# Optimization experiments

Measured on AMD Instinct MI355X. Metric: run time of the kernel, lower is better.

The kernel has to match this reference:

```python
import jax, jax.numpy as jnp
import numpy as np

B, V, H = 16384, 1024, 256


def setup_inputs() -> dict:
    key = jax.random.key(0)
    k1, k2 = jax.random.split(key)
    # binary spin configurations in {0,1}
    batch = jax.random.bernoulli(k1, 0.5, (B, V)).astype(jnp.float32)
    # small weights + negative hidden bias keep exp(log p*) finite in fp32
    weights_amp = jax.random.normal(k2, (H, V), dtype=jnp.float32) * (0.05 / np.sqrt(V))
    visible_bias_amp = jnp.zeros((V,), dtype=jnp.float32)
    hidden_bias_amp = -5.0 * jnp.ones((H,), dtype=jnp.float32)
    return {
        'batch': batch,
        'weights_amp': weights_amp,
        'visible_bias_amp': visible_bias_amp,
        'hidden_bias_amp': hidden_bias_amp,
        'k': 8,
    }


def _gibbs_sampling_amp(v0, W, vb, hb, k, key):
    """k steps of block Gibbs sampling, vectorized over the whole batch [B,V]."""
    keys = jax.random.split(key, 2 * k).reshape(k, 2)

    def step(v, ks):
        ph = jax.nn.sigmoid(v @ W.T + hb)                      # [B,H]
        h = (jax.random.uniform(ks[0], ph.shape) < ph).astype(v.dtype)
        pv = jax.nn.sigmoid(h @ W + vb)                        # [B,V]
        v = (jax.random.uniform(ks[1], pv.shape) < pv).astype(v.dtype)
        return v, None

    vk, _ = jax.lax.scan(step, v0, keys)
    return vk


def reference(batch, weights_amp, visible_bias_amp, hidden_bias_amp, k):
    W, vb, hb = weights_amp, visible_bias_amp, hidden_bias_amp
    nbatch = batch.shape[0]
    key = jax.random.key(42)

    vk = _gibbs_sampling_amp(batch, W, vb, hb, k, key)          # [B,V]

    ph0 = jax.nn.sigmoid(batch @ W.T + hb)                      # [B,H] positive-phase hidden probs
    pre_k = vk @ W.T + hb                                       # [B,H]
    phk = jax.nn.sigmoid(pre_k)                                 # [B,H] negative-phase hidden probs

    # unnormalized_probability_amp(vk) = exp(vk.vb + sum_j softplus((W vk + hb)_j))
    log_p = vk @ vb + jax.nn.softplus(pre_k).sum(axis=-1)       # [B]
    inv_norm = jnp.exp(-log_p) / nbatch                         # 1 / (len(batch) * p*(vk))

    # g_W = sum_b [outer(phk_b, vk_b) - outer(ph0_b, v0_b)] / norm_b
    g_w = (jnp.einsum('b,bh,bv->hv', inv_norm, phk, vk)
           - jnp.einsum('b,bh,bv->hv', inv_norm, ph0, batch))   # [H,V]
    g_vb = jnp.einsum('b,bv->v', inv_norm, vk - batch)          # [V]
    g_hb = jnp.einsum('b,bh->h', inv_norm, phk - ph0)           # [H]

    return jnp.concatenate([g_w.ravel(), g_vb, g_hb])
```

## Files before the change

kernel.cpp:

```cpp
#include <hip/hip_runtime.h>
#include <stdint.h>

#define B_DIM 16384
#define V_DIM 1024
#define H_DIM 256
#define K_STEPS 8

typedef short bf16x8 __attribute__((ext_vector_type(8)));
typedef float f32x4 __attribute__((ext_vector_type(4)));

__host__ __device__ inline uint32_t rotl32(uint32_t v, int r) {
#if defined(__HIP_DEVICE_COMPILE__)
    return __builtin_amdgcn_alignbit(v, v, (uint32_t)(32 - r));
#else
    return (v << r) | (v >> (32 - r));
#endif
}

__host__ __device__ inline void threefry2x32(uint32_t k0, uint32_t k1,
                                             uint32_t x0, uint32_t x1,
                                             uint32_t* o0, uint32_t* o1) {
    uint32_t k2 = k0 ^ k1 ^ 0x1BD11BDAu;
    x0 += k0; x1 += k1;
#define TF_RND(r) { x0 += x1; x1 = rotl32(x1, (r)); x1 ^= x0; }
    TF_RND(13) TF_RND(15) TF_RND(26) TF_RND(6)
    x0 += k1; x1 += k2 + 1u;
    TF_RND(17) TF_RND(29) TF_RND(16) TF_RND(24)
    x0 += k2; x1 += k0 + 2u;
    TF_RND(13) TF_RND(15) TF_RND(26) TF_RND(6)
    x0 += k0; x1 += k1 + 3u;
    TF_RND(17) TF_RND(29) TF_RND(16) TF_RND(24)
    x0 += k1; x1 += k2 + 4u;
    TF_RND(13) TF_RND(15) TF_RND(26) TF_RND(6)
    x0 += k2; x1 += k0 + 5u;
#undef TF_RND
    *o0 = x0; *o1 = x1;
}

__device__ inline float tf_uniform(uint32_t key0, uint32_t key1, uint32_t e) {
    uint32_t o0, o1;
    threefry2x32(key0, key1, 0u, e, &o0, &o1);
    uint32_t bits = o0 ^ o1;
    return __uint_as_float((bits >> 9) | 0x3f800000u) - 1.0f;
}

__device__ inline uint16_t bf16_rn(float f) {
    uint32_t u = __float_as_uint(f);
    uint32_t r = u + 0x7FFFu + ((u >> 16) & 1u);
    return (uint16_t)(r >> 16);
}
__device__ inline float bf16_to_f32(uint16_t h) {
    return __uint_as_float(((uint32_t)h) << 16);
}

__device__ inline void gload_lds16(const void* g, void* l) {
    __builtin_amdgcn_global_load_lds((const __attribute__((address_space(1))) uint32_t*)g,
                                     (__attribute__((address_space(3))) uint32_t*)l, 16, 0, 0);
}

struct KeyPack { uint32_t hk0[8], hk1[8], vk0[8], vk1[8]; };

__global__ __launch_bounds__(512, 4) void gibbs_fused(
    const ushort* __restrict__ batch_bf,
    const ushort* __restrict__ Whi, const ushort* __restrict__ Wlo,
    const float* __restrict__ Wf, const float* __restrict__ vb,
    const float* __restrict__ hb, ushort* __restrict__ v_cur,
    ushort* __restrict__ ph0b, ushort* __restrict__ phkb, KeyPack kp) {
    __shared__ __align__(16) ushort As[2][32 * 32];
    __shared__ __align__(16) ushort BhS[2][256 * 32];
    __shared__ __align__(16) ushort BlS[2][256 * 32];

    const int tid = threadIdx.x;
    const int lane = tid & 63;
    const int w = tid >> 6;
    const int m0 = blockIdx.x * 32;

    const int wm = (w & 1) * 16;
    const int wn = (w >> 1) * 64;
    const int q = lane >> 4;
    const int l15 = lane & 15;
    const int srow = lane >> 2;
    const int scol = (lane & 3) * 8;

    ushort* h_lds = &BhS[0][0];

    for (int step = 0; step <= K_STEPS; ++step) {
        const ushort* Asrc = (step == 0) ? batch_bf : v_cur;
        f32x4 acc[4] = {};

        for (int k0 = 0; k0 < V_DIM; k0 += 64) {
            if (w < 4) {
                const int s = w & 1, rh = w >> 1;
                gload_lds16(&Asrc[(size_t)(m0 + rh * 16 + srow) * V_DIM + k0 + s * 32 + scol],
                            &As[s][rh * 512]);
            }
#pragma unroll
            for (int c = 0; c < 4; ++c) {
                const int cc = w + 8 * c;
                const int s = cc & 1, rb = cc >> 1;
                const size_t off = (size_t)(rb * 16 + srow) * V_DIM + k0 + s * 32 + scol;
                gload_lds16(&Whi[off], &BhS[s][rb * 512]);
                gload_lds16(&Wlo[off], &BlS[s][rb * 512]);
            }
            __syncthreads();
#pragma unroll
            for (int s = 0; s < 2; ++s) {
                bf16x8 af = *(const bf16x8*)&As[s][(wm + l15) * 32 + q * 8];
#pragma unroll
                for (int j = 0; j < 4; ++j) {
                    bf16x8 bh = *(const bf16x8*)&BhS[s][(wn + j * 16 + l15) * 32 + q * 8];
                    bf16x8 bl = *(const bf16x8*)&BlS[s][(wn + j * 16 + l15) * 32 + q * 8];
                    acc[j] = __builtin_amdgcn_mfma_f32_16x16x32_bf16(af, bh, acc[j], 0, 0, 0);
                    acc[j] = __builtin_amdgcn_mfma_f32_16x16x32_bf16(af, bl, acc[j], 0, 0, 0);
                }
            }
            __syncthreads();
        }

        if (step == K_STEPS) {
#pragma unroll
            for (int j = 0; j < 4; ++j) {
                const int col = wn + j * 16 + l15;
                const float hbv = hb[col];
#pragma unroll
                for (int r = 0; r < 4; ++r) {
                    const int row = m0 + wm + q * 4 + r;
                    float val = acc[j][r] + hbv;
                    phkb[(size_t)row * H_DIM + col] = bf16_rn(1.0f / (1.0f + expf(-val)));
                }
            }
            break;
        }

        const uint32_t kh0 = kp.hk0[step], kh1 = kp.hk1[step];
#pragma unroll
        for (int j = 0; j < 4; ++j) {
            const int col = wn + j * 16 + l15;
            const float hbv = hb[col];
#pragma unroll
            for (int r = 0; r < 4; ++r) {
                const int rowl = wm + q * 4 + r;
                const int row = m0 + rowl;
                float val = acc[j][r] + hbv;
                float E = expf(-val);
                float u = tf_uniform(kh0, kh1, (uint32_t)row * (uint32_t)H_DIM + (uint32_t)col);
                h_lds[rowl * H_DIM + col] = (fmaf(u, E, u) < 1.0f) ? (ushort)0x3F80 : (ushort)0;
                if (step == 0) {
                    ph0b[(size_t)row * H_DIM + col] = bf16_rn(1.0f / (1.0f + E));
                }
            }
        }
        __syncthreads();

        const uint32_t kv0 = kp.vk0[step], kv1 = kp.vk1[step];
        float vbr[16];
#pragma unroll
        for (int t = 0; t < 16; ++t) vbr[t] = vb[lane + 64 * t];
#pragma unroll
        for (int rr = 0; rr < 4; ++rr) {
            const int bl_ = w * 4 + rr;
            const int b = m0 + bl_;
            ushort4 hv = ((const ushort4*)(h_lds + bl_ * H_DIM))[lane];
            unsigned long long masks[4];
            masks[0] = __ballot(hv.x != 0);
            masks[1] = __ballot(hv.y != 0);
            masks[2] = __ballot(hv.z != 0);
            masks[3] = __ballot(hv.w != 0);

            float acc2[16];
#pragma unroll
            for (int t = 0; t < 16; ++t) acc2[t] = 0.0f;

#pragma unroll
            for (int s = 0; s < 4; ++s) {
                unsigned long long m = masks[s];
                while (m) {
                    int l = __ffsll(m) - 1;
                    m &= m - 1;
                    int jj = l * 4 + s;
                    const float* wrow = Wf + (size_t)jj * V_DIM + lane;
#pragma unroll
                    for (int t = 0; t < 16; ++t) acc2[t] += wrow[64 * t];
                }
            }

            const uint32_t ebase = (uint32_t)b * (uint32_t)V_DIM + (uint32_t)lane;
            ushort* orow = v_cur + (size_t)b * V_DIM + lane;
#pragma unroll
            for (int t = 0; t < 16; ++t) {
                float pre = acc2[t] + vbr[t];
                float E = expf(-pre);
                float u = tf_uniform(kv0, kv1, ebase + 64u * (uint32_t)t);
                orow[64 * t] = (fmaf(u, E, u) < 1.0f) ? (ushort)0x3F80 : (ushort)0;
            }
        }
        __syncthreads();
    }
}

__global__ __launch_bounds__(256, 4) void mfma_gemm_acc(
    const ushort* __restrict__ A, const ushort* __restrict__ Bt,
    float* __restrict__ out, int N, int K, int k_slice) {
    __shared__ __align__(16) ushort As[64 * 32];
    __shared__ __align__(16) ushort Bs[64 * 32];

    const int tid = threadIdx.x;
    const int lane = tid & 63;
    const int w = tid >> 6;
    const int m0 = blockIdx.x * 64;
    const int n0 = blockIdx.y * 64;
    const int kbase = blockIdx.z * k_slice;

    f32x4 acc[2][2] = {};

    const int wm = (w & 1) * 32;
    const int wn = (w >> 1) * 32;
    const int q = lane >> 4;
    const int l15 = lane & 15;
    const int srow = lane >> 2;
    const int scol = (lane & 3) * 8;

    const size_t arow = (size_t)(m0 + w * 16 + srow) * K;
    const size_t brow = (size_t)(n0 + w * 16 + srow) * K;

    for (int kt = 0; kt < k_slice; kt += 32) {
        const int k0 = kbase + kt;
        gload_lds16(&A[arow + k0 + scol], &As[w * 512]);
        gload_lds16(&Bt[brow + k0 + scol], &Bs[w * 512]);
        __syncthreads();
        bf16x8 af[2], bf[2];
#pragma unroll
        for (int i = 0; i < 2; ++i) {
            af[i] = *(const bf16x8*)&As[(wm + i * 16 + l15) * 32 + q * 8];
            bf[i] = *(const bf16x8*)&Bs[(wn + i * 16 + l15) * 32 + q * 8];
        }
#pragma unroll
        for (int i = 0; i < 2; ++i)
#pragma unroll
            for (int j = 0; j < 2; ++j)
                acc[i][j] = __builtin_amdgcn_mfma_f32_16x16x32_bf16(af[i], bf[j], acc[i][j], 0, 0, 0);
        __syncthreads();
    }

    const int orow = q * 4;
#pragma unroll
    for (int i = 0; i < 2; ++i)
#pragma unroll
        for (int j = 0; j < 2; ++j) {
            int col = n0 + wn + j * 16 + l15;
#pragma unroll
            for (int r = 0; r < 4; ++r) {
                int row = m0 + wm + i * 16 + orow + r;
                atomicAdd(&out[(size_t)row * N + col], acc[i][j][r]);
            }
        }
}

__global__ void wsplit_kernel(const float* __restrict__ W, ushort* __restrict__ whi,
                              ushort* __restrict__ wlo) {
    int idx = blockIdx.x * 256 + threadIdx.x;
    float w = W[idx];
    ushort hi = bf16_rn(w);
    float fhi = bf16_to_f32(hi);
    ushort lo = bf16_rn(w - fhi);
    whi[idx] = hi; wlo[idx] = lo;
}

__global__ void tobf16_kernel(const float* __restrict__ src, ushort* __restrict__ dst) {
    int idx = blockIdx.x * 256 + threadIdx.x;
    float4 f = ((const float4*)src)[idx];
    ushort4 o;
    o.x = bf16_rn(f.x); o.y = bf16_rn(f.y); o.z = bf16_rn(f.z); o.w = bf16_rn(f.w);
    ((ushort4*)dst)[idx] = o;
}

__global__ __launch_bounds__(256) void lognorm_kernel(
    const ushort* __restrict__ phk, const ushort* __restrict__ vk,
    const float* __restrict__ vb, float* __restrict__ inv) {
    int b = blockIdx.x;
    int tid = threadIdx.x;
    float p = bf16_to_f32(phk[(size_t)b * H_DIM + tid]);
    float s = -log1pf(-p);
    for (int j = tid; j < V_DIM; j += 256)
        s += bf16_to_f32(vk[(size_t)b * V_DIM + j]) * vb[j];
    for (int off = 32; off > 0; off >>= 1) s += __shfl_down(s, off, 64);
    __shared__ float wsum[4];
    int lane = tid & 63, wid = tid >> 6;
    if (lane == 0) wsum[wid] = s;
    __syncthreads();
    if (tid == 0) {
        float t = wsum[0] + wsum[1] + wsum[2] + wsum[3];
        inv[b] = expf(-t) * (1.0f / 16384.0f);
    }
}

__global__ void build_At(const ushort* __restrict__ P, const float* __restrict__ inv,
                         float sgn, ushort* __restrict__ At) {
    __shared__ float T[64][65];
    int c = threadIdx.x & 63;
    int rb = threadIdx.x >> 6;
    int b0 = blockIdx.x * 64;
    int h0 = blockIdx.y * 64;
    for (int r = rb; r < 64; r += 4) {
        int b = b0 + r;
        T[c][r] = sgn * inv[b] * bf16_to_f32(P[(size_t)b * H_DIM + h0 + c]);
    }
    __syncthreads();
    for (int r = rb; r < 64; r += 4)
        At[(size_t)(h0 + r) * B_DIM + b0 + c] = bf16_rn(T[r][c]);
}

__global__ void build_Bt(const ushort* __restrict__ Sb, const float* __restrict__ Sf,
                         int use_f32, ushort* __restrict__ Bt) {
    __shared__ ushort T[64][65];
    int c = threadIdx.x & 63;
    int rb = threadIdx.x >> 6;
    int b0 = blockIdx.x * 64;
    int v0 = blockIdx.y * 64;
    for (int r = rb; r < 64; r += 4) {
        int b = b0 + r;
        T[c][r] = use_f32 ? bf16_rn(Sf[(size_t)b * V_DIM + v0 + c])
                          : Sb[(size_t)b * V_DIM + v0 + c];
    }
    __syncthreads();
    for (int r = rb; r < 64; r += 4)
        Bt[(size_t)(v0 + r) * B_DIM + b0 + c] = T[r][c];
}

__global__ void gvb_kernel(const ushort* __restrict__ vk, const ushort* __restrict__ vbat,
                           const float* __restrict__ inv, float* __restrict__ gvb) {
    int col = blockIdx.x * 256 + threadIdx.x;
    int b0 = blockIdx.y * 512;
    float acc = 0.0f;
    for (int r = 0; r < 512; ++r) {
        int b = b0 + r;
        acc += inv[b] * (bf16_to_f32(vk[(size_t)b * V_DIM + col]) -
                         bf16_to_f32(vbat[(size_t)b * V_DIM + col]));
    }
    atomicAdd(&gvb[col], acc);
}

__global__ void ghb_kernel(const ushort* __restrict__ phk, const ushort* __restrict__ ph0,
                           const float* __restrict__ inv, float* __restrict__ ghb) {
    int col = threadIdx.x;
    int b0 = blockIdx.x * 256;
    float acc = 0.0f;
    for (int r = 0; r < 256; ++r) {
        int b = b0 + r;
        acc += inv[b] * (bf16_to_f32(phk[(size_t)b * H_DIM + col]) -
                         bf16_to_f32(ph0[(size_t)b * H_DIM + col]));
    }
    atomicAdd(&ghb[col], acc);
}

extern "C" void kernel_launch(void* const* d_in, const int* in_sizes, int n_in,
                              void* d_out, int out_size, void* d_ws, size_t ws_size,
                              hipStream_t stream) {
    const float* batch = (const float*)d_in[0];
    const float* W = (const float*)d_in[1];
    const float* vb = (const float*)d_in[2];
    const float* hb = (const float*)d_in[3];

    char* base = (char*)d_ws;
    ushort* w_hi  = (ushort*)(base + 0);
    ushort* w_lo  = (ushort*)(base + 524288);
    ushort* v_cur = (ushort*)(base + 2097152);
    float*  inv   = (float*)(base + 35651584);
    ushort* At    = (ushort*)(base + 35717120);
    ushort* batch_bf = (ushort*)(base + 44105728);
    ushort* Bt    = batch_bf;
    ushort* ph0b  = (ushort*)(base + 77660160);
    ushort* phkb  = (ushort*)(base + 86048768);

    float* gw  = (float*)d_out;
    float* gvb = gw + (size_t)H_DIM * V_DIM;
    float* ghb = gvb + V_DIM;

    hipMemsetAsync(d_out, 0, (size_t)out_size * sizeof(float), stream);

    KeyPack kp;
    for (int i = 0; i < K_STEPS; ++i) {
        threefry2x32(0u, 42u, 0u, (uint32_t)(2 * i),     &kp.hk0[i], &kp.hk1[i]);
        threefry2x32(0u, 42u, 0u, (uint32_t)(2 * i + 1), &kp.vk0[i], &kp.vk1[i]);
    }

    wsplit_kernel<<<dim3(1024), dim3(256), 0, stream>>>(W, w_hi, w_lo);
    tobf16_kernel<<<dim3(B_DIM * V_DIM / 4 / 256), dim3(256), 0, stream>>>(batch, batch_bf);

    gibbs_fused<<<dim3(B_DIM / 32), dim3(512), 0, stream>>>(
        batch_bf, w_hi, w_lo, W, vb, hb, v_cur, ph0b, phkb, kp);

    lognorm_kernel<<<dim3(B_DIM), dim3(256), 0, stream>>>(phkb, v_cur, vb, inv);
    ghb_kernel<<<dim3(B_DIM / 256), dim3(256), 0, stream>>>(phkb, ph0b, inv, ghb);
    gvb_kernel<<<dim3(V_DIM / 256, B_DIM / 512), dim3(256), 0, stream>>>(v_cur, batch_bf, inv, gvb);

    build_At<<<dim3(B_DIM / 64, H_DIM / 64), dim3(256), 0, stream>>>(phkb, inv, 1.0f, At);
    build_Bt<<<dim3(B_DIM / 64, V_DIM / 64), dim3(256), 0, stream>>>(v_cur, nullptr, 0, Bt);
    mfma_gemm_acc<<<dim3(H_DIM / 64, V_DIM / 64, 16), dim3(256), 0, stream>>>(
        At, Bt, gw, V_DIM, B_DIM, 1024);
    build_At<<<dim3(B_DIM / 64, H_DIM / 64), dim3(256), 0, stream>>>(ph0b, inv, -1.0f, At);
    build_Bt<<<dim3(B_DIM / 64, V_DIM / 64), dim3(256), 0, stream>>>(nullptr, batch, 1, Bt);
    mfma_gemm_acc<<<dim3(H_DIM / 64, V_DIM / 64, 16), dim3(256), 0, stream>>>(
        At, Bt, gw, V_DIM, B_DIM, 1024);
}
```

Baseline: 917.2 us.

## Interleave RNG generation into GEMM k-loop and swizzle LDS tiles

Threefry uniforms for the hidden sampling and for half of the visible sampling are now computed inside the fully unrolled k-loop, so they can overlap with MFMA work and global-to-LDS loads instead of running serially afterward. The LDS layout is merged into single A and B buffers, with an XOR swizzle applied to source addresses and reads to reduce bank conflicts, and source pointers are precomputed. The cost is 48 extra live registers for the uniforms, which may lower occupancy under the 512x4 launch bounds, plus a longer unrolled loop.

```diff
diff --git a/kernel.cpp b/kernel.cpp
--- a/kernel.cpp
+++ b/kernel.cpp
@@ -66,9 +66,8 @@
     const float* __restrict__ Wf, const float* __restrict__ vb,
     const float* __restrict__ hb, ushort* __restrict__ v_cur,
     ushort* __restrict__ ph0b, ushort* __restrict__ phkb, KeyPack kp) {
-    __shared__ __align__(16) ushort As[2][32 * 32];
-    __shared__ __align__(16) ushort BhS[2][256 * 32];
-    __shared__ __align__(16) ushort BlS[2][256 * 32];
+    __shared__ __align__(16) ushort Am[32 * 64];
+    __shared__ __align__(16) ushort Bm[256 * 128];
 
     const int tid = threadIdx.x;
     const int lane = tid & 63;
@@ -79,39 +78,86 @@
     const int wn = (w >> 1) * 64;
     const int q = lane >> 4;
     const int l15 = lane & 15;
-    const int srow = lane >> 2;
-    const int scol = (lane & 3) * 8;
-
-    ushort* h_lds = &BhS[0][0];
+
+    const ushort* bsrc[8];
+#pragma unroll
+    for (int c = 0; c < 8; ++c) {
+        const int row = w * 32 + c * 4 + (lane >> 4);
+        const int slot = lane & 15;
+        const int us = slot ^ (row & 15);
+        const int hl = (us >> 2) & 1;
+        const int s = us >> 3;
+        const int qq = us & 3;
+        bsrc[c] = (hl ? Wlo : Whi) + (size_t)row * V_DIM + s * 32 + qq * 8;
+    }
+    size_t a_src_off;
+    {
+        const int arow = w * 8 + (lane >> 3);
+        const int aslot = lane & 7;
+        const int us = aslot ^ (arow & 7);
+        const int s = us >> 2;
+        const int qq = us & 3;
+        a_src_off = (size_t)(m0 + arow) * V_DIM + s * 32 + qq * 8;
+    }
+
+    const int arow_ = wm + l15;
+    const int aqxl = (q * 16) ^ ((l15 & 7) << 4);
+    const int qxl = (q * 16) ^ (l15 << 4);
+
+    ushort* h_lds = &Bm[0];
+
+    float uh[16];
+    float uv[32];
 
     for (int step = 0; step <= K_STEPS; ++step) {
         const ushort* Asrc = (step == 0) ? batch_bf : v_cur;
+        uint32_t kh0s = 0, kh1s = 0, kv0s = 0, kv1s = 0;
+        if (step < K_STEPS) {
+            kh0s = kp.hk0[step]; kh1s = kp.hk1[step];
+            kv0s = kp.vk0[step]; kv1s = kp.vk1[step];
+        }
         f32x4 acc[4] = {};
 
-        for (int k0 = 0; k0 < V_DIM; k0 += 64) {
-            if (w < 4) {
-                const int s = w & 1, rh = w >> 1;
-                gload_lds16(&Asrc[(size_t)(m0 + rh * 16 + srow) * V_DIM + k0 + s * 32 + scol],
-                            &As[s][rh * 512]);
-            }
-#pragma unroll
-            for (int c = 0; c < 4; ++c) {
-                const int cc = w + 8 * c;
-                const int s = cc & 1, rb = cc >> 1;
-                const size_t off = (size_t)(rb * 16 + srow) * V_DIM + k0 + s * 32 + scol;
-                gload_lds16(&Whi[off], &BhS[s][rb * 512]);
-                gload_lds16(&Wlo[off], &BlS[s][rb * 512]);
-            }
+#pragma unroll
+        for (int k0i = 0; k0i < 16; ++k0i) {
+            const int k0 = k0i * 64;
+            if (w < 4) gload_lds16(Asrc + a_src_off + k0, &Am[w * 512]);
+#pragma unroll
+            for (int c = 0; c < 8; ++c)
+                gload_lds16(bsrc[c] + k0, &Bm[(w * 8 + c) * 512]);
             __syncthreads();
+
 #pragma unroll
             for (int s = 0; s < 2; ++s) {
-                bf16x8 af = *(const bf16x8*)&As[s][(wm + l15) * 32 + q * 8];
+                bf16x8 af = *(const bf16x8*)((const char*)Am + arow_ * 128 + ((s * 64) ^ aqxl));
 #pragma unroll
                 for (int j = 0; j < 4; ++j) {
-                    bf16x8 bh = *(const bf16x8*)&BhS[s][(wn + j * 16 + l15) * 32 + q * 8];
-                    bf16x8 bl = *(const bf16x8*)&BlS[s][(wn + j * 16 + l15) * 32 + q * 8];
+                    const char* bbase = (const char*)Bm + (wn + j * 16 + l15) * 256;
+                    bf16x8 bh = *(const bf16x8*)(bbase + ((s * 128) ^ qxl));
+                    bf16x8 bl = *(const bf16x8*)(bbase + ((s * 128 + 64) ^ qxl));
                     acc[j] = __builtin_amdgcn_mfma_f32_16x16x32_bf16(af, bh, acc[j], 0, 0, 0);
                     acc[j] = __builtin_amdgcn_mfma_f32_16x16x32_bf16(af, bl, acc[j], 0, 0, 0);
+                }
+            }
+
+            if (step < K_STEPS) {
+#pragma unroll
+                for (int uu = 0; uu < 3; ++uu) {
+                    const int idx = k0i * 3 + uu;
+                    if (idx < 16) {
+                        const int j = idx >> 2, r = idx & 3;
+                        const uint32_t e =
+                            (uint32_t)(m0 + wm + q * 4 + r) * (uint32_t)H_DIM +
+                            (uint32_t)(wn + j * 16 + l15);
+                        uh[idx] = tf_uniform(kh0s, kh1s, e);
+                    } else {
+                        const int iv = idx - 16;
+                        const int rr = iv >> 4, t = iv & 15;
+                        const uint32_t e =
+                            (uint32_t)(m0 + w * 4 + rr) * (uint32_t)V_DIM +
+                            (uint32_t)lane + 64u * (uint32_t)t;
+                        uv[iv] = tf_uniform(kv0s, kv1s, e);
+                    }
                 }
             }
             __syncthreads();
@@ -132,7 +178,6 @@
             break;
         }
 
-        const uint32_t kh0 = kp.hk0[step], kh1 = kp.hk1[step];
 #pragma unroll
         for (int j = 0; j < 4; ++j) {
             const int col = wn + j * 16 + l15;
@@ -143,7 +188,7 @@
                 const int row = m0 + rowl;
                 float val = acc[j][r] + hbv;
                 float E = expf(-val);
-                float u = tf_uniform(kh0, kh1, (uint32_t)row * (uint32_t)H_DIM + (uint32_t)col);
+                float u = uh[j * 4 + r];
                 h_lds[rowl * H_DIM + col] = (fmaf(u, E, u) < 1.0f) ? (ushort)0x3F80 : (ushort)0;
                 if (step == 0) {
                     ph0b[(size_t)row * H_DIM + col] = bf16_rn(1.0f / (1.0f + E));
@@ -152,7 +197,6 @@
         }
         __syncthreads();
 
-        const uint32_t kv0 = kp.vk0[step], kv1 = kp.vk1[step];
         float vbr[16];
 #pragma unroll
         for (int t = 0; t < 16; ++t) vbr[t] = vb[lane + 64 * t];
@@ -190,7 +234,8 @@
             for (int t = 0; t < 16; ++t) {
                 float pre = acc2[t] + vbr[t];
                 float E = expf(-pre);
-                float u = tf_uniform(kv0, kv1, ebase + 64u * (uint32_t)t);
+                float u = (rr < 2) ? uv[rr * 16 + t]
+                                   : tf_uniform(kv0s, kv1s, ebase + 64u * (uint32_t)t);
                 orow[64 * t] = (fmaf(u, E, u) < 1.0f) ? (ushort)0x3F80 : (ushort)0;
             }
         }
```

Result: slower. 1.665 ms (+81.5%).

## Keep visible state as LDS bitmasks and single-buffer swizzled W tiles

Applied to the files above, without the earlier changes.

The visible vector for each block's 32 rows is now kept in LDS as packed bitmasks built with ballots. The bf16 A fragments are rebuilt from these bits, so v no longer round-trips through global memory each Gibbs step; it is written out only on the last step. The W hi/lo tiles are merged into one XOR-swizzled LDS buffer with a K-tile of 32 instead of 64, which doubles the barrier count per GEMM. Launch bounds drop to 2 blocks per CU, possibly trading occupancy for registers.

```diff
diff --git a/kernel.cpp b/kernel.cpp
--- a/kernel.cpp
+++ b/kernel.cpp
@@ -60,15 +60,14 @@
 
 struct KeyPack { uint32_t hk0[8], hk1[8], vk0[8], vk1[8]; };
 
-__global__ __launch_bounds__(512, 4) void gibbs_fused(
+__global__ __launch_bounds__(512, 2) void gibbs_fused(
     const ushort* __restrict__ batch_bf,
     const ushort* __restrict__ Whi, const ushort* __restrict__ Wlo,
     const float* __restrict__ Wf, const float* __restrict__ vb,
     const float* __restrict__ hb, ushort* __restrict__ v_cur,
     ushort* __restrict__ ph0b, ushort* __restrict__ phkb, KeyPack kp) {
-    __shared__ __align__(16) ushort As[2][32 * 32];
-    __shared__ __align__(16) ushort BhS[2][256 * 32];
-    __shared__ __align__(16) ushort BlS[2][256 * 32];
+    __shared__ __align__(16) ushort Bm[256 * 64];
+    __shared__ uint32_t Bv[32 * 32];
 
     const int tid = threadIdx.x;
     const int lane = tid & 63;
@@ -79,40 +78,62 @@
     const int wn = (w >> 1) * 64;
     const int q = lane >> 4;
     const int l15 = lane & 15;
-    const int srow = lane >> 2;
-    const int scol = (lane & 3) * 8;
-
-    ushort* h_lds = &BhS[0][0];
+    const int ra = wm + l15;
+
+    const ushort* bsrc[4];
+#pragma unroll
+    for (int c = 0; c < 4; ++c) {
+        const int row = w * 32 + c * 8 + (lane >> 3);
+        const int sl = (lane & 7) ^ (row & 7);
+        const int hl = sl >> 2;
+        const int qq = sl & 3;
+        bsrc[c] = (hl ? Wlo : Whi) + (size_t)row * V_DIM + qq * 8;
+    }
+
+    ushort* h_lds = &Bm[0];
+
+#pragma unroll
+    for (int rr = 0; rr < 4; ++rr) {
+        const int row = w * 4 + rr;
+        const ushort* brp = batch_bf + (size_t)(m0 + row) * V_DIM;
+#pragma unroll
+        for (int t = 0; t < 16; ++t) {
+            bool dec = brp[lane + 64 * t] != 0;
+            unsigned long long bal = __ballot(dec);
+            if ((lane >> 1) == t) {
+                uint32_t val = (lane & 1) ? (uint32_t)(bal >> 32) : (uint32_t)bal;
+                Bv[row * 32 + ((2 * t + (lane & 1)) ^ (row & 31))] = val;
+            }
+        }
+    }
+    __syncthreads();
 
     for (int step = 0; step <= K_STEPS; ++step) {
-        const ushort* Asrc = (step == 0) ? batch_bf : v_cur;
         f32x4 acc[4] = {};
 
-        for (int k0 = 0; k0 < V_DIM; k0 += 64) {
-            if (w < 4) {
-                const int s = w & 1, rh = w >> 1;
-                gload_lds16(&Asrc[(size_t)(m0 + rh * 16 + srow) * V_DIM + k0 + s * 32 + scol],
-                            &As[s][rh * 512]);
-            }
-#pragma unroll
-            for (int c = 0; c < 4; ++c) {
-                const int cc = w + 8 * c;
-                const int s = cc & 1, rb = cc >> 1;
-                const size_t off = (size_t)(rb * 16 + srow) * V_DIM + k0 + s * 32 + scol;
-                gload_lds16(&Whi[off], &BhS[s][rb * 512]);
-                gload_lds16(&Wlo[off], &BlS[s][rb * 512]);
-            }
+        for (int k0i = 0; k0i < 32; ++k0i) {
+            const int k0 = k0i * 32;
+#pragma unroll
+            for (int c = 0; c < 4; ++c)
+                gload_lds16(bsrc[c] + k0, &Bm[(w * 32 + c * 8) * 64]);
             __syncthreads();
-#pragma unroll
-            for (int s = 0; s < 2; ++s) {
-                bf16x8 af = *(const bf16x8*)&As[s][(wm + l15) * 32 + q * 8];
-#pragma unroll
-                for (int j = 0; j < 4; ++j) {
-                    bf16x8 bh = *(const bf16x8*)&BhS[s][(wn + j * 16 + l15) * 32 + q * 8];
-                    bf16x8 bl = *(const bf16x8*)&BlS[s][(wn + j * 16 + l15) * 32 + q * 8];
-                    acc[j] = __builtin_amdgcn_mfma_f32_16x16x32_bf16(af, bh, acc[j], 0, 0, 0);
-                    acc[j] = __builtin_amdgcn_mfma_f32_16x16x32_bf16(af, bl, acc[j], 0, 0, 0);
-                }
+
+            const uint32_t vw = Bv[ra * 32 + (k0i ^ (ra & 31))];
+            const uint32_t bq = (vw >> (q * 8)) & 0xffu;
+            bf16x8 af;
+#pragma unroll
+            for (int e = 0; e < 8; ++e)
+                af[e] = (short)(((bq >> e) & 1u) ? 0x3F80 : 0);
+
+#pragma unroll
+            for (int j = 0; j < 4; ++j) {
+                const int rb = wn + j * 16 + l15;
+                const char* bb = (const char*)Bm + rb * 128;
+                const int st = (q ^ (rb & 7)) * 16;
+                bf16x8 bh = *(const bf16x8*)(bb + st);
+                bf16x8 bl = *(const bf16x8*)(bb + (st ^ 64));
+                acc[j] = __builtin_amdgcn_mfma_f32_16x16x32_bf16(af, bh, acc[j], 0, 0, 0);
+                acc[j] = __builtin_amdgcn_mfma_f32_16x16x32_bf16(af, bl, acc[j], 0, 0, 0);
             }
             __syncthreads();
         }
@@ -132,7 +153,7 @@
             break;
         }
 
-        const uint32_t kh0 = kp.hk0[step], kh1 = kp.hk1[step];
+        const uint32_t kh0s = kp.hk0[step], kh1s = kp.hk1[step];
 #pragma unroll
         for (int j = 0; j < 4; ++j) {
             const int col = wn + j * 16 + l15;
@@ -143,7 +164,8 @@
                 const int row = m0 + rowl;
                 float val = acc[j][r] + hbv;
                 float E = expf(-val);
-                float u = tf_uniform(kh0, kh1, (uint32_t)row * (uint32_t)H_DIM + (uint32_t)col);
+                float u = tf_uniform(kh0s, kh1s,
+                                     (uint32_t)row * (uint32_t)H_DIM + (uint32_t)col);
                 h_lds[rowl * H_DIM + col] = (fmaf(u, E, u) < 1.0f) ? (ushort)0x3F80 : (ushort)0;
                 if (step == 0) {
                     ph0b[(size_t)row * H_DIM + col] = bf16_rn(1.0f / (1.0f + E));
@@ -152,7 +174,7 @@
         }
         __syncthreads();
 
-        const uint32_t kv0 = kp.vk0[step], kv1 = kp.vk1[step];
+        const uint32_t kv0s = kp.vk0[step], kv1s = kp.vk1[step];
         float vbr[16];
 #pragma unroll
         for (int t = 0; t < 16; ++t) vbr[t] = vb[lane + 64 * t];
@@ -190,8 +212,14 @@
             for (int t = 0; t < 16; ++t) {
                 float pre = acc2[t] + vbr[t];
                 float E = expf(-pre);
-                float u = tf_uniform(kv0, kv1, ebase + 64u * (uint32_t)t);
-                orow[64 * t] = (fmaf(u, E, u) < 1.0f) ? (ushort)0x3F80 : (ushort)0;
+                float u = tf_uniform(kv0s, kv1s, ebase + 64u * (uint32_t)t);
+                bool dec = (fmaf(u, E, u) < 1.0f);
+                if (step == K_STEPS - 1) orow[64 * t] = dec ? (ushort)0x3F80 : (ushort)0;
+                unsigned long long bal = __ballot(dec);
+                if ((lane >> 1) == t) {
+                    uint32_t val = (lane & 1) ? (uint32_t)(bal >> 32) : (uint32_t)bal;
+                    Bv[bl_ * 32 + ((2 * t + (lane & 1)) ^ (bl_ & 31))] = val;
+                }
             }
         }
         __syncthreads();
```

After: 1.261 ms. +37.5%, slower.
